# Performance work log

Hardware: AMD Instinct MI355X
Metric: run time of the kernel (lower is better)

Reference implementation:

```python
import jax, jax.numpy as jnp
import numpy as np

N_NODES = 50000
N_EDGES = 600000
IN_DIM = 128
HID = 128


def gcn_conv(x, W, b, src, dst, num_nodes):
    """PyG-style GCNConv: add self-loops, symmetric D^-1/2 (A+I) D^-1/2 normalization."""
    xw = x @ W  # [N, H]
    loop = jnp.arange(num_nodes)
    s = jnp.concatenate([src, loop])
    d = jnp.concatenate([dst, loop])
    deg = jax.ops.segment_sum(jnp.ones_like(d, dtype=xw.dtype), d, num_segments=num_nodes)
    dinv = jax.lax.rsqrt(deg)  # deg >= 1 thanks to self-loops
    norm = dinv[s] * dinv[d]  # [E+N]
    msgs = xw[s] * norm[:, None]  # gather + scale, [E+N, H]
    out = jax.ops.segment_sum(msgs, d, num_segments=num_nodes)
    return out + b


def setup_inputs() -> dict:
    key = jax.random.key(0)
    ks = jax.random.split(key, 12)
    sc_in = 1.0 / np.sqrt(IN_DIM)
    sc_h = 1.0 / np.sqrt(HID)
    sc_2h = 1.0 / np.sqrt(2 * HID)
    return {
        "x": jax.random.normal(ks[0], (N_NODES, IN_DIM), jnp.float32),
        "hidden_state": jax.random.normal(ks[1], (N_NODES, HID), jnp.float32),
        "edge_index": jax.random.randint(ks[2], (2, N_EDGES), 0, N_NODES, dtype=jnp.int32),
        "W_in": jax.random.normal(ks[3], (IN_DIM, HID), jnp.float32) * sc_in,
        "b_in": jnp.zeros((HID,), jnp.float32),
        "W_hid": jax.random.normal(ks[4], (HID, HID), jnp.float32) * sc_h,
        "b_hid": jnp.zeros((HID,), jnp.float32),
        "W_z": jax.random.normal(ks[5], (2 * HID, HID), jnp.float32) * sc_2h,
        "b_z": jnp.zeros((HID,), jnp.float32),
        "W_r": jax.random.normal(ks[6], (2 * HID, HID), jnp.float32) * sc_2h,
        "b_r": jnp.zeros((HID,), jnp.float32),
        "W_c": jax.random.normal(ks[7], (2 * HID, HID), jnp.float32) * sc_2h,
        "b_c": jnp.zeros((HID,), jnp.float32),
    }


def reference(x, hidden_state, edge_index, W_in, b_in, W_hid, b_hid, W_z, b_z, W_r, b_r, W_c, b_c):
    src, dst = edge_index[0], edge_index[1]
    n = x.shape[0]
    # two stacked GCN layers (dropout identity in eval mode)
    h1 = jax.nn.relu(gcn_conv(x, W_in, b_in, src, dst, n))
    emb = gcn_conv(h1, W_hid, b_hid, src, dst, n)  # [N, H]
    # GRU-style gating
    combined = jnp.concatenate([emb, hidden_state], axis=1)  # [N, 2H]
    update = jax.nn.sigmoid(combined @ W_z + b_z)
    reset = jax.nn.sigmoid(combined @ W_r + b_r)
    cand_in = jnp.concatenate([emb, reset * hidden_state], axis=1)
    candidate = jnp.tanh(cand_in @ W_c + b_c)
    new_hidden = (1.0 - update) * hidden_state + update * candidate
    return new_hidden
```

## Files before the change

### kernel.cpp

```cpp
#include <hip/hip_runtime.h>
#include <cstdint>
#include <cstddef>

typedef unsigned short u16;
typedef unsigned int   u32;

typedef __bf16 bf8   __attribute__((ext_vector_type(8)));
typedef float  f32x4 __attribute__((ext_vector_type(4)));

__device__ __forceinline__ float b2f(u16 v) {
  union { u32 i; float f; } c; c.i = ((u32)v) << 16; return c.f;
}
__device__ __forceinline__ u16 f2b(float f) {
  union { u32 i; float f; } c; c.f = f;
  u32 x = c.i;
  u32 r = (x + 0x7FFFu + ((x >> 16) & 1u)) >> 16;
  return (u16)r;
}
__device__ __forceinline__ float sigf(float x) { return 1.0f / (1.0f + __expf(-x)); }
__device__ __forceinline__ float tanhfast(float x) { return 2.0f * sigf(2.0f * x) - 1.0f; }

__device__ __forceinline__ bf8 cvt8(const float* __restrict__ p) {
  f32x4 lo = *(const f32x4*)p;
  f32x4 hi = *(const f32x4*)(p + 4);
  union { u16 s[8]; bf8 v; } c;
#pragma unroll
  for (int i = 0; i < 4; ++i) { c.s[i] = f2b(lo[i]); c.s[4 + i] = f2b(hi[i]); }
  return c.v;
}
__device__ __forceinline__ bf8 asbf8(uint4 q) {
  union { uint4 q; bf8 v; } c; c.q = q; return c.v;
}

__device__ __forceinline__ void ld_lds16(const u16* g, u16* l) {
  __builtin_amdgcn_global_load_lds((const __attribute__((address_space(1))) void*)g,
                                   (__attribute__((address_space(3))) void*)l, 16, 0, 0);
}

#define CSR_STRIDE 80

__global__ __launch_bounds__(256) void k_transpose(
    const float* __restrict__ W0, const float* __restrict__ W1,
    const float* __restrict__ W2, const float* __restrict__ W3,
    const float* __restrict__ W4,
    u16* __restrict__ B0, u16* __restrict__ B1, u16* __restrict__ B2,
    u16* __restrict__ B3, u16* __restrict__ B4,
    int* __restrict__ cnt, int N) {
  if (blockIdx.x >= 64) {
    int i = (blockIdx.x - 64) * 256 + threadIdx.x;
    if (i < N) cnt[i] = 0;
    return;
  }
  int t = blockIdx.x * 256 + threadIdx.x;
  const float* in; u16* out; int f;
  if (t < 2048)       { in = W0; out = B0; f = t; }
  else if (t < 4096)  { in = W1; out = B1; f = t - 2048; }
  else if (t < 8192)  { in = W2; out = B2; f = t - 4096; }
  else if (t < 12288) { in = W3; out = B3; f = t - 8192; }
  else                { in = W4; out = B4; f = t - 12288; }
  int ln = f & 15, quad = (f >> 4) & 3, c = (f >> 6) & 7, ks = (f >> 9) & 3, hh = f >> 11;
  int n = c * 16 + ln;
  int k0 = hh * 128 + ks * 32 + quad * 8;
  union { u16 s[8]; uint4 q; } tmp;
#pragma unroll
  for (int j = 0; j < 8; ++j) tmp.s[j] = f2b(in[(size_t)(k0 + j) * 128 + n]);
  *(uint4*)(out + (size_t)f * 8) = tmp.q;
}

__global__ void k_fill(const int* __restrict__ src, const int* __restrict__ dst,
                       int* __restrict__ cnt, int* __restrict__ csr, int E) {
  int e = blockIdx.x * 256 + threadIdx.x;
  if (e < E) {
    int d = dst[e];
    int pos = atomicAdd(&cnt[d], 1);
    if (pos < CSR_STRIDE) csr[(size_t)d * CSR_STRIDE + pos] = src[e];
  }
}

__global__ __launch_bounds__(256) void k_agg(const u16* __restrict__ y,
                                             const int* __restrict__ cnt,
                                             const int* __restrict__ csr,
                                             const float* __restrict__ bias,
                                             u16* __restrict__ out, int relu, int N) {
  int wv = (blockIdx.x * 256 + threadIdx.x) >> 6;
  int lane = threadIdx.x & 63;
  if (wv >= N) return;
  int g = lane >> 4, t = lane & 15;
  const uint4* yq = (const uint4*)y;
  int deg = cnt[wv];
  int degc = (deg < 64) ? deg : 64;
  long base = (long)wv * CSR_STRIDE;
  int myidx = (lane < degc) ? csr[base + lane] : 0;

  float a[8];
#pragma unroll
  for (int j = 0; j < 8; ++j) a[j] = 0.0f;

  for (int b = 0; b < degc; b += 8) {
    int e0 = b + g, e1 = b + 4 + g;
    int s0 = __shfl(myidx, (e0 < degc) ? e0 : 0, 64);
    int s1 = __shfl(myidx, (e1 < degc) ? e1 : 0, 64);
    uint4 v0 = yq[(size_t)s0 * 16 + t];
    uint4 v1 = yq[(size_t)s1 * 16 + t];
    if (e0 < degc) {
      const u32* w = (const u32*)&v0;
#pragma unroll
      for (int i = 0; i < 4; ++i) { a[2*i] += b2f((u16)(w[i] & 0xFFFF)); a[2*i+1] += b2f((u16)(w[i] >> 16)); }
    }
    if (e1 < degc) {
      const u32* w = (const u32*)&v1;
#pragma unroll
      for (int i = 0; i < 4; ++i) { a[2*i] += b2f((u16)(w[i] & 0xFFFF)); a[2*i+1] += b2f((u16)(w[i] >> 16)); }
    }
  }
#pragma unroll
  for (int j = 0; j < 8; ++j) {
    a[j] += __shfl_xor(a[j], 16, 64);
    a[j] += __shfl_xor(a[j], 32, 64);
  }
  if (g == 0) {
    int degt = (deg < CSR_STRIDE) ? deg : CSR_STRIDE;
    for (int p = 64; p < degt; ++p) {
      int s = csr[base + p];
      uint4 v = yq[(size_t)s * 16 + t];
      const u32* w = (const u32*)&v;
#pragma unroll
      for (int i = 0; i < 4; ++i) { a[2*i] += b2f((u16)(w[i] & 0xFFFF)); a[2*i+1] += b2f((u16)(w[i] >> 16)); }
    }
    uint4 sv = yq[(size_t)wv * 16 + t];
    const u32* w = (const u32*)&sv;
#pragma unroll
    for (int i = 0; i < 4; ++i) { a[2*i] += b2f((u16)(w[i] & 0xFFFF)); a[2*i+1] += b2f((u16)(w[i] >> 16)); }
    float di = rsqrtf((float)deg + 1.0f);
    f32x4 b0 = *(const f32x4*)(bias + t * 8);
    f32x4 b1 = *(const f32x4*)(bias + t * 8 + 4);
    union { u16 s[8]; uint4 q; } o;
#pragma unroll
    for (int j = 0; j < 8; ++j) {
      float r = di * a[j] + ((j < 4) ? b0[j] : b1[j - 4]);
      if (relu) r = fmaxf(r, 0.0f);
      o.s[j] = f2b(r);
    }
    ((uint4*)out)[(size_t)wv * 16 + t] = o.q;
  }
}

template <bool AF>
__global__ __launch_bounds__(256) void k_gemm(
    const void* __restrict__ Av,
    const u16* __restrict__ Bt,
    const int* __restrict__ cnt,
    u16* __restrict__ outb, int M) {
  __shared__ __align__(16) u16 bs[16384];
  int tid = threadIdx.x;
  int lane = tid & 63, wave = tid >> 6;
  int ln = lane & 15, quad = lane >> 4;
  int rowbase = blockIdx.x * 64 + wave * 16;
  int rowA = rowbase + ln;
  long rA = (rowA < M) ? rowA : (M - 1);

  {
    const u16* g = Bt + wave * 4096 + lane * 8;
    u16* l = bs + wave * 4096;
#pragma unroll
    for (int i = 0; i < 8; ++i) ld_lds16(g + i * 512, l + i * 512);
  }

  bf8 af[4];
#pragma unroll
  for (int ks = 0; ks < 4; ++ks) {
    int kk = ks * 32 + quad * 8;
    if (AF) af[ks] = cvt8((const float*)Av + rA * 128 + kk);
    else    af[ks] = *(const bf8*)((const u16*)Av + rA * 128 + kk);
  }

  f32x4 acc[8];
#pragma unroll
  for (int c = 0; c < 8; ++c) { acc[c][0] = 0.f; acc[c][1] = 0.f; acc[c][2] = 0.f; acc[c][3] = 0.f; }

  __syncthreads();
#pragma unroll
  for (int ks = 0; ks < 4; ++ks) {
#pragma unroll
    for (int c = 0; c < 8; ++c) {
      bf8 bfr = *(const bf8*)(bs + ks * 4096 + c * 512 + lane * 8);
      acc[c] = __builtin_amdgcn_mfma_f32_16x16x32_bf16(af[ks], bfr, acc[c], 0, 0, 0);
    }
  }

  int rb = rowbase + quad * 4;
  float rs[4];
#pragma unroll
  for (int r = 0; r < 4; ++r) {
    int row = rb + r;
    rs[r] = (row < M) ? rsqrtf((float)cnt[row] + 1.0f) : 0.0f;
  }
#pragma unroll
  for (int c = 0; c < 8; ++c) {
    int col = c * 16 + ln;
#pragma unroll
    for (int r = 0; r < 4; ++r) {
      int row = rb + r;
      if (row < M) outb[(size_t)row * 128 + col] = f2b(acc[c][r] * rs[r]);
    }
  }
}

__global__ __launch_bounds__(256, 2) void k_gru(
    const u16* __restrict__ emb, const float* __restrict__ h,
    const u16* __restrict__ Btz, const u16* __restrict__ Btr, const u16* __restrict__ Btc,
    const float* __restrict__ bz, const float* __restrict__ br, const float* __restrict__ bc,
    float* __restrict__ out, int M) {
  __shared__ __align__(16) u16 at[8192];
  int tid = threadIdx.x;
  int lane = tid & 63, wave = tid >> 6;
  int ln = lane & 15, quad = lane >> 4;
  int rowbase = blockIdx.x * 64 + wave * 16;
  int rowA = rowbase + ln;
  long rA = (rowA < M) ? rowA : (M - 1);
  int rb = rowbase + quad * 4;

  const uint4* Bz = (const uint4*)Btz;
  const uint4* Br = (const uint4*)Btr;
  const uint4* Bc = (const uint4*)Btc;

  bf8 af_e[4], af_h[4];
#pragma unroll
  for (int ks = 0; ks < 4; ++ks)
    af_e[ks] = *(const bf8*)(emb + rA * 128 + ks * 32 + quad * 8);
#pragma unroll
  for (int ks = 0; ks < 4; ++ks)
    af_h[ks] = cvt8(h + rA * 128 + ks * 32 + quad * 8);

  f32x4 accz[8], accr[8];
#pragma unroll
  for (int c = 0; c < 8; ++c) {
    accz[c][0] = 0.f; accz[c][1] = 0.f; accz[c][2] = 0.f; accz[c][3] = 0.f;
    accr[c][0] = 0.f; accr[c][1] = 0.f; accr[c][2] = 0.f; accr[c][3] = 0.f;
  }

  auto loadb = [&](uint4 (&d)[8], const uint4* B, int ksg) {
#pragma unroll
    for (int c = 0; c < 8; ++c) d[c] = B[(size_t)ksg * 512 + c * 64 + lane];
  };
  auto mmzr = [&](uint4 (&cz)[8], uint4 (&cr)[8], int ksg) {
    bf8 af = (ksg < 4) ? af_e[ksg] : af_h[ksg - 4];
#pragma unroll
    for (int c = 0; c < 8; ++c) {
      accz[c] = __builtin_amdgcn_mfma_f32_16x16x32_bf16(af, asbf8(cz[c]), accz[c], 0, 0, 0);
      accr[c] = __builtin_amdgcn_mfma_f32_16x16x32_bf16(af, asbf8(cr[c]), accr[c], 0, 0, 0);
    }
  };

  uint4 z0[8], r0[8], z1[8], r1[8];
  loadb(z0, Bz, 0); loadb(r0, Br, 0);
  loadb(z1, Bz, 1); loadb(r1, Br, 1);
  mmzr(z0, r0, 0);
  loadb(z0, Bz, 2); loadb(r0, Br, 2);
  mmzr(z1, r1, 1);
  loadb(z1, Bz, 3); loadb(r1, Br, 3);
  mmzr(z0, r0, 2);
  loadb(z0, Bz, 4); loadb(r0, Br, 4);
  mmzr(z1, r1, 3);
  loadb(z1, Bz, 5); loadb(r1, Br, 5);
  mmzr(z0, r0, 4);
  loadb(z0, Bz, 6); loadb(r0, Br, 6);
  mmzr(z1, r1, 5);
  loadb(z1, Bz, 7); loadb(r1, Br, 7);
  mmzr(z0, r0, 6);
  mmzr(z1, r1, 7);

  f32x4 hc[8];
#pragma unroll
  for (int c = 0; c < 8; ++c) {
    int col = c * 16 + ln;
#pragma unroll
    for (int r = 0; r < 4; ++r) {
      int row = rb + r;
      hc[c][r] = (row < M) ? h[(size_t)row * 128 + col] : 0.0f;
    }
  }

#pragma unroll
  for (int c = 0; c < 8; ++c) {
    int col = c * 16 + ln;
    float bzc = bz[col], brc = br[col];
#pragma unroll
    for (int r = 0; r < 4; ++r) {
      float uu = sigf(accz[c][r] + bzc);
      float rr = sigf(accr[c][r] + brc);
      accz[c][r] = uu;
      int lrow = wave * 16 + quad * 4 + r;
      at[lrow * 128 + col] = f2b(rr * hc[c][r]);
      accr[c][r] = 0.0f;
    }
  }
  __syncthreads();

  bf8 af_at[4];
#pragma unroll
  for (int ks = 0; ks < 4; ++ks)
    af_at[ks] = *(const bf8*)(at + (wave * 16 + ln) * 128 + ks * 32 + quad * 8);

  auto mmc = [&](uint4 (&cc)[8], int ksg) {
    bf8 af = (ksg < 4) ? af_e[ksg] : af_at[ksg - 4];
#pragma unroll
    for (int c = 0; c < 8; ++c)
      accr[c] = __builtin_amdgcn_mfma_f32_16x16x32_bf16(af, asbf8(cc[c]), accr[c], 0, 0, 0);
  };
  uint4 c0[8], c1[8];
  loadb(c0, Bc, 0);
  loadb(c1, Bc, 1);
  mmc(c0, 0);
  loadb(c0, Bc, 2);
  mmc(c1, 1);
  loadb(c1, Bc, 3);
  mmc(c0, 2);
  loadb(c0, Bc, 4);
  mmc(c1, 3);
  loadb(c1, Bc, 5);
  mmc(c0, 4);
  loadb(c0, Bc, 6);
  mmc(c1, 5);
  loadb(c1, Bc, 7);
  mmc(c0, 6);
  mmc(c1, 7);

#pragma unroll
  for (int c = 0; c < 8; ++c) {
    int col = c * 16 + ln;
    float bcc = bc[col];
#pragma unroll
    for (int r = 0; r < 4; ++r) {
      int row = rb + r;
      if (row < M) {
        float cd = tanhfast(accr[c][r] + bcc);
        float uu = accz[c][r];
        out[(size_t)row * 128 + col] = (1.0f - uu) * hc[c][r] + uu * cd;
      }
    }
  }
}

extern "C" void kernel_launch(void* const* d_in, const int* in_sizes, int n_in,
                              void* d_out, int out_size, void* d_ws, size_t ws_size,
                              hipStream_t stream) {
  const float* x     = (const float*)d_in[0];
  const float* h     = (const float*)d_in[1];
  const int*   ei    = (const int*)d_in[2];
  const float* W_in  = (const float*)d_in[3];
  const float* b_in  = (const float*)d_in[4];
  const float* W_hid = (const float*)d_in[5];
  const float* b_hid = (const float*)d_in[6];
  const float* W_z   = (const float*)d_in[7];
  const float* b_z   = (const float*)d_in[8];
  const float* W_r   = (const float*)d_in[9];
  const float* b_r   = (const float*)d_in[10];
  const float* W_c   = (const float*)d_in[11];
  const float* b_c   = (const float*)d_in[12];

  const int N = in_sizes[0] / 128;
  const int E = in_sizes[2] / 2;
  const int* src = ei;
  const int* dst = ei + E;

  char* p = (char*)d_ws;
  auto carve = [&](size_t bytes) { char* r = p; p += (bytes + 255) & ~(size_t)255; return r; };
  u16* Bt_in   = (u16*)carve((size_t)16384 * 2);
  u16* Bt_hid  = (u16*)carve((size_t)16384 * 2);
  u16* Bt_z    = (u16*)carve((size_t)32768 * 2);
  u16* Bt_r    = (u16*)carve((size_t)32768 * 2);
  u16* Bt_c    = (u16*)carve((size_t)32768 * 2);
  int* cnt  = (int*)carve((size_t)N * 4);
  int* csr  = (int*)carve((size_t)N * CSR_STRIDE * 4);
  u16* y    = (u16*)carve((size_t)N * 128 * 2);
  u16* h1   = (u16*)carve((size_t)N * 128 * 2);
  u16* emb  = (u16*)carve((size_t)N * 128 * 2);

  int gN = (N + 255) / 256;
  int gE = (E + 255) / 256;
  int gG = (N + 63) / 64;
  int gA = (N + 3) / 4;

  k_transpose<<<64 + gN, 256, 0, stream>>>(W_in, W_hid, W_z, W_r, W_c,
                                           Bt_in, Bt_hid, Bt_z, Bt_r, Bt_c, cnt, N);
  k_fill<<<gE, 256, 0, stream>>>(src, dst, cnt, csr, E);

  k_gemm<true><<<gG, 256, 0, stream>>>(x, Bt_in, cnt, y, N);
  k_agg<<<gA, 256, 0, stream>>>(y, cnt, csr, b_in, h1, 1, N);
  k_gemm<false><<<gG, 256, 0, stream>>>(h1, Bt_hid, cnt, y, N);
  k_agg<<<gA, 256, 0, stream>>>(y, cnt, csr, b_hid, emb, 0, N);
  k_gru<<<gG, 256, 0, stream>>>(emb, h, Bt_z, Bt_r, Bt_c, b_z, b_r, b_c, (float*)d_out, N);
}
```

Measured before the change: 267.6 us.

## Stage GRU weight fragments through double-buffered LDS shared by all waves

In the GRU kernel, each wave used to load the z/r/c weight fragments from global memory into registers on its own, so the four waves of a block fetched the same weights redundantly. The weights are now copied once per block with direct global-to-LDS loads into a two-slot ring, with the next k-slice prefetched while MFMAs consume the current one, and all waves read fragments from LDS. This cuts redundant global/L2 traffic and register pressure. In exchange it adds 32KB of LDS per block and a block barrier every k-step, which may limit occupancy and add sync stalls.

```diff
diff --git a/kernel.cpp b/kernel.cpp
--- a/kernel.cpp
+++ b/kernel.cpp
@@ -27,9 +27,6 @@
 #pragma unroll
   for (int i = 0; i < 4; ++i) { c.s[i] = f2b(lo[i]); c.s[4 + i] = f2b(hi[i]); }
   return c.v;
-}
-__device__ __forceinline__ bf8 asbf8(uint4 q) {
-  union { uint4 q; bf8 v; } c; c.q = q; return c.v;
 }
 
 __device__ __forceinline__ void ld_lds16(const u16* g, u16* l) {
@@ -211,6 +208,7 @@
     const u16* __restrict__ Btz, const u16* __restrict__ Btr, const u16* __restrict__ Btc,
     const float* __restrict__ bz, const float* __restrict__ br, const float* __restrict__ bc,
     float* __restrict__ out, int M) {
+  __shared__ __align__(16) u16 ring[2][8192];
   __shared__ __align__(16) u16 at[8192];
   int tid = threadIdx.x;
   int lane = tid & 63, wave = tid >> 6;
@@ -220,9 +218,23 @@
   long rA = (rowA < M) ? rowA : (M - 1);
   int rb = rowbase + quad * 4;
 
-  const uint4* Bz = (const uint4*)Btz;
-  const uint4* Br = (const uint4*)Btr;
-  const uint4* Bc = (const uint4*)Btc;
+  auto stage_zr = [&](int k, int s) {
+#pragma unroll
+    for (int i = 0; i < 2; ++i) {
+      int off = (wave * 2 + i) * 512;
+      ld_lds16(Btz + k * 4096 + off + lane * 8, &ring[s][off]);
+      ld_lds16(Btr + k * 4096 + off + lane * 8, &ring[s][4096 + off]);
+    }
+  };
+  auto stage_c = [&](int k, int s) {
+#pragma unroll
+    for (int i = 0; i < 2; ++i) {
+      int off = (wave * 2 + i) * 512;
+      ld_lds16(Btc + k * 4096 + off + lane * 8, &ring[s][off]);
+    }
+  };
+
+  stage_zr(0, 0);
 
   bf8 af_e[4], af_h[4];
 #pragma unroll
@@ -239,36 +251,24 @@
     accr[c][0] = 0.f; accr[c][1] = 0.f; accr[c][2] = 0.f; accr[c][3] = 0.f;
   }
 
-  auto loadb = [&](uint4 (&d)[8], const uint4* B, int ksg) {
-#pragma unroll
-    for (int c = 0; c < 8; ++c) d[c] = B[(size_t)ksg * 512 + c * 64 + lane];
-  };
-  auto mmzr = [&](uint4 (&cz)[8], uint4 (&cr)[8], int ksg) {
-    bf8 af = (ksg < 4) ? af_e[ksg] : af_h[ksg - 4];
+  __syncthreads();
+
+#pragma unroll
+  for (int k = 0; k < 8; ++k) {
+    if (k < 7) stage_zr(k + 1, (k + 1) & 1);
+    bf8 af = (k < 4) ? af_e[k] : af_h[k - 4];
+    int s = k & 1;
 #pragma unroll
     for (int c = 0; c < 8; ++c) {
-      accz[c] = __builtin_amdgcn_mfma_f32_16x16x32_bf16(af, asbf8(cz[c]), accz[c], 0, 0, 0);
-      accr[c] = __builtin_amdgcn_mfma_f32_16x16x32_bf16(af, asbf8(cr[c]), accr[c], 0, 0, 0);
-    }
-  };
-
-  uint4 z0[8], r0[8], z1[8], r1[8];
-  loadb(z0, Bz, 0); loadb(r0, Br, 0);
-  loadb(z1, Bz, 1); loadb(r1, Br, 1);
-  mmzr(z0, r0, 0);
-  loadb(z0, Bz, 2); loadb(r0, Br, 2);
-  mmzr(z1, r1, 1);
-  loadb(z1, Bz, 3); loadb(r1, Br, 3);
-  mmzr(z0, r0, 2);
-  loadb(z0, Bz, 4); loadb(r0, Br, 4);
-  mmzr(z1, r1, 3);
-  loadb(z1, Bz, 5); loadb(r1, Br, 5);
-  mmzr(z0, r0, 4);
-  loadb(z0, Bz, 6); loadb(r0, Br, 6);
-  mmzr(z1, r1, 5);
-  loadb(z1, Bz, 7); loadb(r1, Br, 7);
-  mmzr(z0, r0, 6);
-  mmzr(z1, r1, 7);
+      bf8 bz_ = *(const bf8*)(&ring[s][(c * 64 + lane) * 8]);
+      bf8 br_ = *(const bf8*)(&ring[s][4096 + (c * 64 + lane) * 8]);
+      accz[c] = __builtin_amdgcn_mfma_f32_16x16x32_bf16(af, bz_, accz[c], 0, 0, 0);
+      accr[c] = __builtin_amdgcn_mfma_f32_16x16x32_bf16(af, br_, accr[c], 0, 0, 0);
+    }
+    __syncthreads();
+  }
+
+  stage_c(0, 0);
 
   f32x4 hc[8];
 #pragma unroll
@@ -302,29 +302,18 @@
   for (int ks = 0; ks < 4; ++ks)
     af_at[ks] = *(const bf8*)(at + (wave * 16 + ln) * 128 + ks * 32 + quad * 8);
 
-  auto mmc = [&](uint4 (&cc)[8], int ksg) {
-    bf8 af = (ksg < 4) ? af_e[ksg] : af_at[ksg - 4];
-#pragma unroll
-    for (int c = 0; c < 8; ++c)
-      accr[c] = __builtin_amdgcn_mfma_f32_16x16x32_bf16(af, asbf8(cc[c]), accr[c], 0, 0, 0);
-  };
-  uint4 c0[8], c1[8];
-  loadb(c0, Bc, 0);
-  loadb(c1, Bc, 1);
-  mmc(c0, 0);
-  loadb(c0, Bc, 2);
-  mmc(c1, 1);
-  loadb(c1, Bc, 3);
-  mmc(c0, 2);
-  loadb(c0, Bc, 4);
-  mmc(c1, 3);
-  loadb(c1, Bc, 5);
-  mmc(c0, 4);
-  loadb(c0, Bc, 6);
-  mmc(c1, 5);
-  loadb(c1, Bc, 7);
-  mmc(c0, 6);
-  mmc(c1, 7);
+#pragma unroll
+  for (int j = 0; j < 8; ++j) {
+    if (j < 7) stage_c(j + 1, (j + 1) & 1);
+    bf8 af = (j < 4) ? af_e[j] : af_at[j - 4];
+    int s = j & 1;
+#pragma unroll
+    for (int c = 0; c < 8; ++c) {
+      bf8 bfr = *(const bf8*)(&ring[s][(c * 64 + lane) * 8]);
+      accr[c] = __builtin_amdgcn_mfma_f32_16x16x32_bf16(af, bfr, accr[c], 0, 0, 0);
+    }
+    if (j < 7) __syncthreads();
+  }
 
 #pragma unroll
   for (int c = 0; c < 8; ++c) {
```

Result: no change. 262.9 us (-1.8%).
